# Kernel tuning notes

Measured on AMD Instinct MI355X. Metric: run time of the kernel, lower is better.

The kernel has to match this reference:

```python
import jax, jax.numpy as jnp
import numpy as np


def setup_inputs() -> dict:
    key = jax.random.key(0)
    k0, k1, k2, k3 = jax.random.split(key, 4)
    B, C_IN, H, W = 8, 256, 64, 64
    O, NUM = 256, 8  # output channels, number of regions
    mat0 = jax.random.normal(k0, (B, C_IN, H, W), dtype=jnp.float32)
    mat1 = jax.random.normal(k1, (O, C_IN, NUM), dtype=jnp.float32)  # per-region 1x1 filters (shared across batch, batch_W=1)
    mask = jax.random.uniform(k2, (NUM, H, W), dtype=jnp.float32)    # soft region weights per pixel
    Alpha = jax.random.uniform(k3, (NUM,), dtype=jnp.float32)        # per-region modulation scale
    return {"mat0": mat0, "mat1": mat1, "mask": mask, "Alpha": Alpha, "use_alpha": 1, "beta": 1}


def reference(mat0, mat1, mask, Alpha, use_alpha, beta):
    # Deformable (region-aware) matmul: for each pixel (h,w), apply the
    # region-r filter mat1[:, :, r] to mat0[:, :, h, w], weighted by the
    # per-pixel soft region mask (optionally alpha-modulated per region).
    # out[b,o,h,w] = sum_r sum_c mat0[b,c,h,w] * mat1[o,c,r] * Alpha[r] * mask[r,h,w]
    m1 = mat1 * Alpha if use_alpha else mat1  # [O, C, R] scaled per region
    return jnp.einsum('bchw,ocr,rhw->bohw', mat0, m1, mask)
```

## Files before the change

### kernel.cpp

```cpp
#include <hip/hip_runtime.h>
#include <hip/hip_bf16.h>
#include <stdint.h>


typedef __attribute__((ext_vector_type(8)))  _Float16 half8;
typedef __attribute__((ext_vector_type(16))) float    f32x16;

#define C_IN  256
#define HW_   4096
#define NRND  32

__global__ __launch_bounds__(256) void prep_w_kernel(
    const float* __restrict__ mat1, const float* __restrict__ Alpha,
    const int* __restrict__ use_alpha, _Float16* __restrict__ Aprep) {
  int t = blockIdx.x * 256 + threadIdx.x;
  int o = t & 255;
  int c = t >> 8;
  int ua = use_alpha[0];
  const float* src = mat1 + ((size_t)o * C_IN + c) * 8;
  half8 v;
#pragma unroll
  for (int r = 0; r < 8; ++r) {
    float s = ua ? Alpha[r] : 1.0f;
    v[r] = (_Float16)(src[r] * s);
  }
  *(half8*)(Aprep + ((size_t)c * 256 + o) * 8) = v;
}

__global__ __launch_bounds__(256, 2) void gemm_deform_kernel(
    const float* __restrict__ mat0, const _Float16* __restrict__ Aprep,
    const float* __restrict__ mask, float* __restrict__ out) {
  __shared__ half8 A_lds[2][1024];

  int bid = blockIdx.x;
  int wg = (bid & 7) * 64 + (bid >> 3);
  int tile_m = wg & 1;
  int tile_n = wg >> 1;
  int o0 = tile_m * 128;
  int n0 = tile_n * 128;
  int b  = n0 >> 12;
  int p0 = n0 & 4095;

  int t    = threadIdx.x;
  int lane = t & 63;
  int w    = t >> 6;
  int wc   = w & 1;
  int wr   = w >> 1;
  int l31  = lane & 31;
  int cr   = lane >> 5;

  int colb = p0 + wc * 64 + l31;
  half8 mkh[2];
#pragma unroll
  for (int ni = 0; ni < 2; ++ni)
#pragma unroll
    for (int r = 0; r < 8; ++r)
      mkh[ni][r] = (_Float16)mask[r * HW_ + colb + ni * 32];

  const float* __restrict__ m0b =
      mat0 + ((size_t)b * C_IN + cr) * HW_ + colb;

  const __attribute__((address_space(1))) uint32_t* gA =
      (const __attribute__((address_space(1))) uint32_t*)Aprep;
  int soo  = (w & 1) * 64 + lane;
  int scqb = w >> 1;

  f32x16 acc[2][2];
#pragma unroll
  for (int mi = 0; mi < 2; ++mi)
#pragma unroll
    for (int ni = 0; ni < 2; ++ni)
#pragma unroll
      for (int j = 0; j < 16; ++j) acc[mi][ni][j] = 0.f;

  float P0[4][2], P1[4][2];

  auto STAGE = [&](int rd, int buf) {
    __attribute__((address_space(3))) uint32_t* lA =
        (__attribute__((address_space(3))) uint32_t*)&A_lds[buf][0];
#pragma unroll
    for (int i = 0; i < 4; ++i) {
      int gslot = (rd * 8 + i * 2 + scqb) * 256 + o0 + soo;
      __builtin_amdgcn_global_load_lds(gA + (size_t)gslot * 4,
                                       lA + (size_t)(i * 256 + w * 64) * 4,
                                       16, 0, 0);
    }
  };

  auto LOADP = [&](float (&P)[4][2], int rd) {
    const float* mp = m0b + (size_t)(rd * 8) * HW_;
#pragma unroll
    for (int kq = 0; kq < 4; ++kq) {
      P[kq][0] = mp[(size_t)(kq * 2) * HW_];
      P[kq][1] = mp[(size_t)(kq * 2) * HW_ + 32];
    }
  };

  auto COMP = [&](const half8* __restrict__ Abuf, float (&P)[4][2], int rd) {
    int rp = rd + 2 > 31 ? 31 : rd + 2;
    const float* mnext = m0b + (size_t)(rp * 8) * HW_;
#pragma unroll
    for (int kq = 0; kq < 4; ++kq) {
      half8 a0 = Abuf[(kq * 2 + cr) * 128 + wr * 64 + l31];
      half8 a1 = Abuf[(kq * 2 + cr) * 128 + wr * 64 + 32 + l31];
      _Float16 h0 = (_Float16)P[kq][0];
      _Float16 h1 = (_Float16)P[kq][1];
      half8 pb0 = {h0, h0, h0, h0, h0, h0, h0, h0};
      half8 pb1 = {h1, h1, h1, h1, h1, h1, h1, h1};
      half8 bv0 = pb0 * mkh[0];
      half8 bv1 = pb1 * mkh[1];
      acc[0][0] = __builtin_amdgcn_mfma_f32_32x32x16_f16(a0, bv0, acc[0][0], 0, 0, 0);
      acc[0][1] = __builtin_amdgcn_mfma_f32_32x32x16_f16(a0, bv1, acc[0][1], 0, 0, 0);
      acc[1][0] = __builtin_amdgcn_mfma_f32_32x32x16_f16(a1, bv0, acc[1][0], 0, 0, 0);
      acc[1][1] = __builtin_amdgcn_mfma_f32_32x32x16_f16(a1, bv1, acc[1][1], 0, 0, 0);
      P[kq][0] = mnext[(size_t)(kq * 2) * HW_];
      P[kq][1] = mnext[(size_t)(kq * 2) * HW_ + 32];
    }
  };

  STAGE(0, 0);
  LOADP(P0, 0);
  LOADP(P1, 1);
  asm volatile("s_waitcnt vmcnt(16)" ::: "memory");
  __builtin_amdgcn_s_barrier();

#pragma unroll 1
  for (int rd = 0; rd < NRND; rd += 2) {
    STAGE(rd + 1, 1);
    COMP(&A_lds[0][0], P0, rd);
    asm volatile("s_waitcnt vmcnt(8)" ::: "memory");
    __builtin_amdgcn_s_barrier();
    if (rd + 2 < NRND) STAGE(rd + 2, 0);
    COMP(&A_lds[1][0], P1, rd + 1);
    asm volatile("s_waitcnt vmcnt(8)" ::: "memory");
    __builtin_amdgcn_s_barrier();
  }

  size_t obase = (size_t)b * 256 * HW_ + colb;
#pragma unroll
  for (int mi = 0; mi < 2; ++mi) {
#pragma unroll
    for (int ni = 0; ni < 2; ++ni) {
#pragma unroll
      for (int reg = 0; reg < 16; ++reg) {
        int row = o0 + wr * 64 + mi * 32 + (reg & 3) + 8 * (reg >> 2) + 4 * cr;
        out[obase + (size_t)row * HW_ + ni * 32] = acc[mi][ni][reg];
      }
    }
  }
}

extern "C" void kernel_launch(void* const* d_in, const int* in_sizes, int n_in,
                              void* d_out, int out_size, void* d_ws, size_t ws_size,
                              hipStream_t stream) {
  const float* mat0      = (const float*)d_in[0];
  const float* mat1      = (const float*)d_in[1];
  const float* mask      = (const float*)d_in[2];
  const float* Alpha     = (const float*)d_in[3];
  const int*   use_alpha = (const int*)d_in[4];
  (void)in_sizes; (void)n_in; (void)out_size; (void)ws_size;

  _Float16* Aprep = (_Float16*)d_ws;
  float* outp  = (float*)d_out;

  prep_w_kernel<<<256, 256, 0, stream>>>(mat1, Alpha, use_alpha, Aprep);
  gemm_deform_kernel<<<512, 256, 0, stream>>>(mat0, Aprep, mask, outp);
}
```

Before: 48.13 us.

## Use wave-private LDS staging for weights and drop workgroup barriers

```diff
diff --git a/kernel.cpp b/kernel.cpp
--- a/kernel.cpp
+++ b/kernel.cpp
@@ -30,7 +30,7 @@
 __global__ __launch_bounds__(256, 2) void gemm_deform_kernel(
     const float* __restrict__ mat0, const _Float16* __restrict__ Aprep,
     const float* __restrict__ mask, float* __restrict__ out) {
-  __shared__ half8 A_lds[2][1024];
+  __shared__ half8 A_lds[2][4][512];
 
   int bid = blockIdx.x;
   int wg = (bid & 7) * 64 + (bid >> 3);
@@ -62,8 +62,9 @@
 
   const __attribute__((address_space(1))) uint32_t* gA =
       (const __attribute__((address_space(1))) uint32_t*)Aprep;
-  int soo  = (w & 1) * 64 + lane;
-  int scqb = w >> 1;
+  __attribute__((address_space(3))) uint32_t* lA =
+      (__attribute__((address_space(3))) uint32_t*)&A_lds[0][0][0];
+  int arow = o0 + wr * 64 + lane;
 
   f32x16 acc[2][2];
 #pragma unroll
@@ -76,14 +77,12 @@
   float P0[4][2], P1[4][2];
 
   auto STAGE = [&](int rd, int buf) {
-    __attribute__((address_space(3))) uint32_t* lA =
-        (__attribute__((address_space(3))) uint32_t*)&A_lds[buf][0];
 #pragma unroll
-    for (int i = 0; i < 4; ++i) {
-      int gslot = (rd * 8 + i * 2 + scqb) * 256 + o0 + soo;
+    for (int i = 0; i < 8; ++i) {
+      int gslot = (rd * 8 + i) * 256 + arow;
+      int lslot = (buf * 4 + w) * 512 + i * 64;
       __builtin_amdgcn_global_load_lds(gA + (size_t)gslot * 4,
-                                       lA + (size_t)(i * 256 + w * 64) * 4,
-                                       16, 0, 0);
+                                       lA + (size_t)lslot * 4, 16, 0, 0);
     }
   };
 
@@ -101,39 +100,40 @@
     const float* mnext = m0b + (size_t)(rp * 8) * HW_;
 #pragma unroll
     for (int kq = 0; kq < 4; ++kq) {
-      half8 a0 = Abuf[(kq * 2 + cr) * 128 + wr * 64 + l31];
-      half8 a1 = Abuf[(kq * 2 + cr) * 128 + wr * 64 + 32 + l31];
+      half8 a0 = Abuf[(kq * 2 + cr) * 64 + l31];
+      half8 a1 = Abuf[(kq * 2 + cr) * 64 + 32 + l31];
       _Float16 h0 = (_Float16)P[kq][0];
       _Float16 h1 = (_Float16)P[kq][1];
       half8 pb0 = {h0, h0, h0, h0, h0, h0, h0, h0};
       half8 pb1 = {h1, h1, h1, h1, h1, h1, h1, h1};
       half8 bv0 = pb0 * mkh[0];
       half8 bv1 = pb1 * mkh[1];
+      __builtin_amdgcn_s_setprio(1);
       acc[0][0] = __builtin_amdgcn_mfma_f32_32x32x16_f16(a0, bv0, acc[0][0], 0, 0, 0);
       acc[0][1] = __builtin_amdgcn_mfma_f32_32x32x16_f16(a0, bv1, acc[0][1], 0, 0, 0);
       acc[1][0] = __builtin_amdgcn_mfma_f32_32x32x16_f16(a1, bv0, acc[1][0], 0, 0, 0);
       acc[1][1] = __builtin_amdgcn_mfma_f32_32x32x16_f16(a1, bv1, acc[1][1], 0, 0, 0);
+      __builtin_amdgcn_s_setprio(0);
       P[kq][0] = mnext[(size_t)(kq * 2) * HW_];
       P[kq][1] = mnext[(size_t)(kq * 2) * HW_ + 32];
     }
   };
 
+  const half8* buf0 = &A_lds[0][0][0] + w * 512;
+  const half8* buf1 = &A_lds[1][0][0] + w * 512;
+
   STAGE(0, 0);
   LOADP(P0, 0);
   LOADP(P1, 1);
-  asm volatile("s_waitcnt vmcnt(16)" ::: "memory");
-  __builtin_amdgcn_s_barrier();
 
 #pragma unroll 1
   for (int rd = 0; rd < NRND; rd += 2) {
     STAGE(rd + 1, 1);
-    COMP(&A_lds[0][0], P0, rd);
-    asm volatile("s_waitcnt vmcnt(8)" ::: "memory");
-    __builtin_amdgcn_s_barrier();
-    if (rd + 2 < NRND) STAGE(rd + 2, 0);
-    COMP(&A_lds[1][0], P1, rd + 1);
-    asm volatile("s_waitcnt vmcnt(8)" ::: "memory");
-    __builtin_amdgcn_s_barrier();
+    asm volatile("s_waitcnt vmcnt(16)" ::: "memory");
+    COMP(buf0, P0, rd);
+    STAGE(rd + 2 > 31 ? 31 : rd + 2, 0);
+    asm volatile("s_waitcnt vmcnt(16)" ::: "memory");
+    COMP(buf1, P1, rd + 1);
   }
 
   size_t obase = (size_t)b * 256 * HW_ + colb;
```

After: 54.08 us. 12.4% more time.

## Restructure GEMM main loop to single-round prefetch with interleaved LDS staging

Applied to the files above, without the earlier changes.

```diff
diff --git a/kernel.cpp b/kernel.cpp
--- a/kernel.cpp
+++ b/kernel.cpp
@@ -62,6 +62,8 @@
 
   const __attribute__((address_space(1))) uint32_t* gA =
       (const __attribute__((address_space(1))) uint32_t*)Aprep;
+  __attribute__((address_space(3))) uint32_t* lA =
+      (__attribute__((address_space(3))) uint32_t*)&A_lds[0][0];
   int soo  = (w & 1) * 64 + lane;
   int scqb = w >> 1;
 
@@ -73,66 +75,55 @@
 #pragma unroll
       for (int j = 0; j < 16; ++j) acc[mi][ni][j] = 0.f;
 
-  float P0[4][2], P1[4][2];
+  float P[4][2];
 
-  auto STAGE = [&](int rd, int buf) {
-    __attribute__((address_space(3))) uint32_t* lA =
-        (__attribute__((address_space(3))) uint32_t*)&A_lds[buf][0];
 #pragma unroll
-    for (int i = 0; i < 4; ++i) {
-      int gslot = (rd * 8 + i * 2 + scqb) * 256 + o0 + soo;
+  for (int i = 0; i < 4; ++i) {
+    int gslot = (0 * 8 + i * 2 + scqb) * 256 + o0 + soo;
+    __builtin_amdgcn_global_load_lds(gA + (size_t)gslot * 4,
+                                     lA + (size_t)(i * 256 + w * 64) * 4,
+                                     16, 0, 0);
+  }
+#pragma unroll
+  for (int kq = 0; kq < 4; ++kq) {
+    P[kq][0] = m0b[(size_t)(kq * 2) * HW_];
+    P[kq][1] = m0b[(size_t)(kq * 2) * HW_ + 32];
+  }
+  asm volatile("s_waitcnt vmcnt(8)" ::: "memory");
+  __builtin_amdgcn_s_barrier();
+
+#pragma unroll 1
+  for (int rd = 0; rd < NRND; ++rd) {
+    const half8* __restrict__ Abuf = &A_lds[rd & 1][0];
+    int bufn = (rd & 1) ^ 1;
+    int rs = rd + 1 > 31 ? 31 : rd + 1;
+    int gbase = rs * 8;
+#pragma unroll
+    for (int p = 0; p < 4; ++p) {
+      int gslot = (gbase + p * 2 + scqb) * 256 + o0 + soo;
       __builtin_amdgcn_global_load_lds(gA + (size_t)gslot * 4,
-                                       lA + (size_t)(i * 256 + w * 64) * 4,
+                                       lA + (size_t)(bufn * 1024 + p * 256 + w * 64) * 4,
                                        16, 0, 0);
-    }
-  };
-
-  auto LOADP = [&](float (&P)[4][2], int rd) {
-    const float* mp = m0b + (size_t)(rd * 8) * HW_;
-#pragma unroll
-    for (int kq = 0; kq < 4; ++kq) {
-      P[kq][0] = mp[(size_t)(kq * 2) * HW_];
-      P[kq][1] = mp[(size_t)(kq * 2) * HW_ + 32];
-    }
-  };
-
-  auto COMP = [&](const half8* __restrict__ Abuf, float (&P)[4][2], int rd) {
-    int rp = rd + 2 > 31 ? 31 : rd + 2;
-    const float* mnext = m0b + (size_t)(rp * 8) * HW_;
-#pragma unroll
-    for (int kq = 0; kq < 4; ++kq) {
-      half8 a0 = Abuf[(kq * 2 + cr) * 128 + wr * 64 + l31];
-      half8 a1 = Abuf[(kq * 2 + cr) * 128 + wr * 64 + 32 + l31];
-      _Float16 h0 = (_Float16)P[kq][0];
-      _Float16 h1 = (_Float16)P[kq][1];
+      half8 a0 = Abuf[(p * 2 + cr) * 128 + wr * 64 + l31];
+      half8 a1 = Abuf[(p * 2 + cr) * 128 + wr * 64 + 32 + l31];
+      __builtin_amdgcn_s_barrier();
+      _Float16 h0 = (_Float16)P[p][0];
+      _Float16 h1 = (_Float16)P[p][1];
       half8 pb0 = {h0, h0, h0, h0, h0, h0, h0, h0};
       half8 pb1 = {h1, h1, h1, h1, h1, h1, h1, h1};
       half8 bv0 = pb0 * mkh[0];
       half8 bv1 = pb1 * mkh[1];
+      __builtin_amdgcn_s_setprio(1);
       acc[0][0] = __builtin_amdgcn_mfma_f32_32x32x16_f16(a0, bv0, acc[0][0], 0, 0, 0);
       acc[0][1] = __builtin_amdgcn_mfma_f32_32x32x16_f16(a0, bv1, acc[0][1], 0, 0, 0);
       acc[1][0] = __builtin_amdgcn_mfma_f32_32x32x16_f16(a1, bv0, acc[1][0], 0, 0, 0);
       acc[1][1] = __builtin_amdgcn_mfma_f32_32x32x16_f16(a1, bv1, acc[1][1], 0, 0, 0);
-      P[kq][0] = mnext[(size_t)(kq * 2) * HW_];
-      P[kq][1] = mnext[(size_t)(kq * 2) * HW_ + 32];
+      __builtin_amdgcn_s_setprio(0);
+      const float* mnext = m0b + (size_t)(gbase + p * 2) * HW_;
+      P[p][0] = mnext[0];
+      P[p][1] = mnext[32];
     }
-  };
-
-  STAGE(0, 0);
-  LOADP(P0, 0);
-  LOADP(P1, 1);
-  asm volatile("s_waitcnt vmcnt(16)" ::: "memory");
-  __builtin_amdgcn_s_barrier();
-
-#pragma unroll 1
-  for (int rd = 0; rd < NRND; rd += 2) {
-    STAGE(rd + 1, 1);
-    COMP(&A_lds[0][0], P0, rd);
-    asm volatile("s_waitcnt vmcnt(8)" ::: "memory");
-    __builtin_amdgcn_s_barrier();
-    if (rd + 2 < NRND) STAGE(rd + 2, 0);
-    COMP(&A_lds[1][0], P1, rd + 1);
-    asm volatile("s_waitcnt vmcnt(8)" ::: "memory");
+    asm volatile("s_waitcnt vmcnt(2)" ::: "memory");
     __builtin_amdgcn_s_barrier();
   }
 
```

After: 50.68 us. +5.3%, slower.

## Deepen LDS pipeline to four slabs, add MFMA priority and staggered k-order

Applied to the files above, without the earlier changes.

```diff
diff --git a/kernel.cpp b/kernel.cpp
--- a/kernel.cpp
+++ b/kernel.cpp
@@ -30,7 +30,7 @@
 __global__ __launch_bounds__(256, 2) void gemm_deform_kernel(
     const float* __restrict__ mat0, const _Float16* __restrict__ Aprep,
     const float* __restrict__ mask, float* __restrict__ out) {
-  __shared__ half8 A_lds[2][1024];
+  __shared__ half8 A_lds[4][1024];
 
   int bid = blockIdx.x;
   int wg = (bid & 7) * 64 + (bid >> 3);
@@ -62,6 +62,8 @@
 
   const __attribute__((address_space(1))) uint32_t* gA =
       (const __attribute__((address_space(1))) uint32_t*)Aprep;
+  __attribute__((address_space(3))) uint32_t* lA =
+      (__attribute__((address_space(3))) uint32_t*)&A_lds[0][0];
   int soo  = (w & 1) * 64 + lane;
   int scqb = w >> 1;
 
@@ -73,16 +75,14 @@
 #pragma unroll
       for (int j = 0; j < 16; ++j) acc[mi][ni][j] = 0.f;
 
-  float P0[4][2], P1[4][2];
+  float PA[4][2], PB[4][2], PC[4][2], PD[4][2];
 
-  auto STAGE = [&](int rd, int buf) {
-    __attribute__((address_space(3))) uint32_t* lA =
-        (__attribute__((address_space(3))) uint32_t*)&A_lds[buf][0];
+  auto STAGE = [&](int rd, int s) {
 #pragma unroll
     for (int i = 0; i < 4; ++i) {
       int gslot = (rd * 8 + i * 2 + scqb) * 256 + o0 + soo;
       __builtin_amdgcn_global_load_lds(gA + (size_t)gslot * 4,
-                                       lA + (size_t)(i * 256 + w * 64) * 4,
+                                       lA + (size_t)(s * 1024 + i * 256 + w * 64) * 4,
                                        16, 0, 0);
     }
   };
@@ -96,45 +96,61 @@
     }
   };
 
-  auto COMP = [&](const half8* __restrict__ Abuf, float (&P)[4][2], int rd) {
-    int rp = rd + 2 > 31 ? 31 : rd + 2;
-    const float* mnext = m0b + (size_t)(rp * 8) * HW_;
-#pragma unroll
-    for (int kq = 0; kq < 4; ++kq) {
-      half8 a0 = Abuf[(kq * 2 + cr) * 128 + wr * 64 + l31];
-      half8 a1 = Abuf[(kq * 2 + cr) * 128 + wr * 64 + 32 + l31];
-      _Float16 h0 = (_Float16)P[kq][0];
-      _Float16 h1 = (_Float16)P[kq][1];
-      half8 pb0 = {h0, h0, h0, h0, h0, h0, h0, h0};
-      half8 pb1 = {h1, h1, h1, h1, h1, h1, h1, h1};
-      half8 bv0 = pb0 * mkh[0];
-      half8 bv1 = pb1 * mkh[1];
-      acc[0][0] = __builtin_amdgcn_mfma_f32_32x32x16_f16(a0, bv0, acc[0][0], 0, 0, 0);
-      acc[0][1] = __builtin_amdgcn_mfma_f32_32x32x16_f16(a0, bv1, acc[0][1], 0, 0, 0);
-      acc[1][0] = __builtin_amdgcn_mfma_f32_32x32x16_f16(a1, bv0, acc[1][0], 0, 0, 0);
-      acc[1][1] = __builtin_amdgcn_mfma_f32_32x32x16_f16(a1, bv1, acc[1][1], 0, 0, 0);
-      P[kq][0] = mnext[(size_t)(kq * 2) * HW_];
-      P[kq][1] = mnext[(size_t)(kq * 2) * HW_ + 32];
-    }
+#define KQ_STEP(KQ) do {                                                      \
+    half8 a0 = Abuf[((KQ) * 2 + cr) * 128 + wr * 64 + l31];                   \
+    half8 a1 = Abuf[((KQ) * 2 + cr) * 128 + wr * 64 + 32 + l31];              \
+    _Float16 h0 = (_Float16)P[KQ][0];                                         \
+    _Float16 h1 = (_Float16)P[KQ][1];                                         \
+    half8 pb0 = {h0, h0, h0, h0, h0, h0, h0, h0};                             \
+    half8 pb1 = {h1, h1, h1, h1, h1, h1, h1, h1};                             \
+    half8 bv0 = pb0 * mkh[0];                                                 \
+    half8 bv1 = pb1 * mkh[1];                                                 \
+    __builtin_amdgcn_s_setprio(1);                                            \
+    acc[0][0] = __builtin_amdgcn_mfma_f32_32x32x16_f16(a0, bv0, acc[0][0], 0, 0, 0); \
+    acc[0][1] = __builtin_amdgcn_mfma_f32_32x32x16_f16(a0, bv1, acc[0][1], 0, 0, 0); \
+    acc[1][0] = __builtin_amdgcn_mfma_f32_32x32x16_f16(a1, bv0, acc[1][0], 0, 0, 0); \
+    acc[1][1] = __builtin_amdgcn_mfma_f32_32x32x16_f16(a1, bv1, acc[1][1], 0, 0, 0); \
+    __builtin_amdgcn_s_setprio(0);                                            \
+  } while (0)
+
+  auto comp0 = [&](const half8* __restrict__ Abuf, const float (&P)[4][2]) {
+    KQ_STEP(0); KQ_STEP(1); KQ_STEP(2); KQ_STEP(3);
+  };
+  auto comp2 = [&](const half8* __restrict__ Abuf, const float (&P)[4][2]) {
+    KQ_STEP(2); KQ_STEP(3); KQ_STEP(0); KQ_STEP(1);
   };
 
-  STAGE(0, 0);
-  LOADP(P0, 0);
-  LOADP(P1, 1);
-  asm volatile("s_waitcnt vmcnt(16)" ::: "memory");
-  __builtin_amdgcn_s_barrier();
+  const half8* __restrict__ slab0 = &A_lds[0][0];
+  const half8* __restrict__ slab1 = &A_lds[1][0];
+  const half8* __restrict__ slab2 = &A_lds[2][0];
+  const half8* __restrict__ slab3 = &A_lds[3][0];
 
-#pragma unroll 1
-  for (int rd = 0; rd < NRND; rd += 2) {
-    STAGE(rd + 1, 1);
-    COMP(&A_lds[0][0], P0, rd);
-    asm volatile("s_waitcnt vmcnt(8)" ::: "memory");
-    __builtin_amdgcn_s_barrier();
-    if (rd + 2 < NRND) STAGE(rd + 2, 0);
-    COMP(&A_lds[1][0], P1, rd + 1);
-    asm volatile("s_waitcnt vmcnt(8)" ::: "memory");
-    __builtin_amdgcn_s_barrier();
+  STAGE(0, 0); STAGE(1, 1);
+  LOADP(PA, 0); LOADP(PB, 1);
+
+#define MAIN_LOOP(COMPF)                                                      \
+  _Pragma("unroll 1")                                                         \
+  for (int i = 0; i < 8; ++i) {                                               \
+    int r0 = i * 4;                                                           \
+      \
+    asm volatile("s_waitcnt vmcnt(0)" ::: "memory");                          \
+    __builtin_amdgcn_s_barrier();                                             \
+    STAGE(r0 + 2, 2); STAGE(r0 + 3, 3);                                       \
+    LOADP(PC, r0 + 2); LOADP(PD, r0 + 3);                                     \
+    COMPF(slab0, PA); COMPF(slab1, PB);                                       \
+    \
+    asm volatile("s_waitcnt vmcnt(0)" ::: "memory");                          \
+    __builtin_amdgcn_s_barrier();                                             \
+    {                                                                         \
+      int r4 = r0 + 4 > 31 ? 31 : r0 + 4;            \
+      int r5 = r0 + 5 > 31 ? 31 : r0 + 5;                                     \
+      STAGE(r4, 0); STAGE(r5, 1);                                             \
+      LOADP(PA, r4); LOADP(PB, r5);                                           \
+    }                                                                         \
+    COMPF(slab2, PC); COMPF(slab3, PD);                                       \
   }
+
+  if (bid & 1) { MAIN_LOOP(comp2) } else { MAIN_LOOP(comp0) }
 
   size_t obase = (size_t)b * 256 * HW_ + colb;
 #pragma unroll
```

Measured after the change: 50.63 us. +5.2%, slower.
